# Kernel tuning notes

Measured on AMD Instinct MI355X. Metric: run time of the kernel, lower is better.

## Reference

```python
import jax, jax.numpy as jnp
import numpy as np

SPIN_LEN = 365
TRAIN_LEN = 200000
ML = 2.9086  # mean of second forcing (hard-coded in the torch module)
SL = 1.898   # std of second forcing (hard-coded in the torch module)


def setup_inputs() -> dict:
    key = jax.random.key(0)
    kx, ky, kp = jax.random.split(key, 3)
    B, S = 262144, 1
    x = jax.random.uniform(kx, (B, S, 2), dtype=jnp.float32)
    y_obs = jax.random.uniform(ky, (B, 1), dtype=jnp.float32)
    ks = jax.random.split(kp, 6)
    return {
        "x": x,
        "y_obs": y_obs,
        "epoch": 1,
        "time_lag": 0,
        "weight_r_yom": jax.random.uniform(ks[0], (1, 1), dtype=jnp.float32),
        "weight_r_yom_gw": jax.random.uniform(ks[1], (1, 1), dtype=jnp.float32),
        "weight_r_ylm": jax.random.uniform(ks[2], (1, 1), dtype=jnp.float32),
        "weight_r_yfm": jax.random.uniform(ks[3], (1, 1), dtype=jnp.float32),
        "bias_b0_ylm": jax.random.uniform(ks[4], (1,), dtype=jnp.float32),
        "weight_b2_ylm": jax.random.uniform(ks[5], (1, 1), dtype=jnp.float32),
    }


def reference(x, y_obs, epoch, time_lag, weight_r_yom, weight_r_yom_gw,
              weight_r_ylm, weight_r_yfm, bias_b0_ylm, weight_b2_ylm):
    # x: [B, S, 2] (batch_first). The torch code transposes to [S, B, 2] and
    # runs b-outer / t-inner loops with state threaded across BOTH loops, so
    # the scan order over flattened steps is b-major, t-minor.
    B, S, _ = x.shape
    dt = x.dtype

    # softmax-like mass-balance gate normalization over the 4 scalar weights
    e_om = jnp.exp(weight_r_yom[0, 0])
    e_gw = jnp.exp(weight_r_yom_gw[0, 0])
    e_lm = jnp.exp(weight_r_ylm[0, 0])
    e_fm = jnp.exp(weight_r_yfm[0, 0])
    denom = e_om + e_gw + e_lm + e_fm
    oo = e_om / denom      # constant output gate
    oogw = e_gw / denom    # constant groundwater gate
    ol1 = e_lm / denom     # loss-gate scale
    b0 = bias_b0_ylm[0]
    wb2 = weight_b2_ylm[0, 0]

    # unbiased std, matching torch.std default
    obsstd = jnp.std(y_obs[SPIN_LEN:TRAIN_LEN], ddof=1)

    xv = x[time_lag:]                       # [B', S, 2] (time_lag is static)
    Bp = B - time_lag
    u1 = xv[..., 0].reshape(-1)             # [B'*S] inflow
    u2 = xv[..., 1].reshape(-1)             # [B'*S] loss forcing

    def step(c, u):
        u1_t, u2_t = u
        ol = ol1 * jax.nn.sigmoid(b0 + (u2_t - ML) / SL * wb2)
        f = 1.0 - oo - ol - oogw
        c_new = f * c + u1_t                # ib = 0 -> full inflow enters
        return c_new, (c, ol, f)

    _, (c_prev, ol_s, f_s) = jax.lax.scan(step, jnp.zeros((), dt), (u1, u2))

    # torch stores outputs every t but overwrites; only last t per b survives,
    # using c_0 (state BEFORE that step) and that step's ol/f.
    c0 = c_prev.reshape(Bp, S)[:, -1]
    olL = ol_s.reshape(Bp, S)[:, -1]
    fL = f_s.reshape(Bp, S)[:, -1]

    def pad(v):  # rows b < time_lag stay zero, shape [B, 1]
        return jnp.pad(v, (time_lag, 0))[:, None]

    h_n = pad(oo * c0)          # bp = 0 so h_n == q_n
    c_n = pad(c0)
    l_n = pad(olL * c0)
    gw_n = pad(oogw * c0)
    bp_n = jnp.zeros((B, 1), dt)
    gate_ib = jnp.zeros((B, 1), dt)
    valid = pad(jnp.ones((Bp,), dt))
    gate_oo = oo * valid
    gate_oogw = oogw * valid
    gate_ol = pad(olL)
    gate_f = pad(fL)
    obs_std = obsstd * valid
    h_nout = jnp.concatenate([h_n, obs_std], axis=1)
    return (h_n, c_n, l_n, gw_n, bp_n, gate_ib, gate_oo, gate_oogw,
            gate_ol, gate_f, h_nout, obs_std)
```

## Files before the change

kernel.cpp:

```cpp
#include <hip/hip_runtime.h>
#include <math.h>

#define SPIN 365
#define TRAINL 200000

#define THREADS 256
#define ITEMS 4
#define CHUNK (THREADS * ITEMS)


struct Sc { float oo, oogw, ol1, b0, wb2; };

__device__ __forceinline__ Sc get_sc(const float* w0, const float* w1,
                                     const float* w2, const float* w3,
                                     const float* b0p, const float* wb2p) {
  float e_om = expf(w0[0]);
  float e_gw = expf(w1[0]);
  float e_lm = expf(w2[0]);
  float e_fm = expf(w3[0]);
  float denom = e_om + e_gw + e_lm + e_fm;
  Sc s;
  s.oo   = e_om / denom;
  s.oogw = e_gw / denom;
  s.ol1  = e_lm / denom;
  s.b0   = b0p[0];
  s.wb2  = wb2p[0];
  return s;
}

__device__ __forceinline__ float sigm(float z) { return 1.0f / (1.0f + expf(-z)); }


extern "C" __global__ __launch_bounds__(THREADS) void k_phase1(
    const float* __restrict__ x, const float* __restrict__ y,
    const int* __restrict__ tlp,
    const float* __restrict__ w0, const float* __restrict__ w1,
    const float* __restrict__ w2, const float* __restrict__ w3,
    const float* __restrict__ b0p, const float* __restrict__ wb2p,
    float* __restrict__ out, float* __restrict__ ws, int B, int G)
{
  const int g = blockIdx.x, tid = threadIdx.x;
  const int tl = tlp[0];
  const Sc sc = get_sc(w0, w1, w2, w3, b0p, wb2p);
  const int base = g * CHUNK + tid * ITEMS;
  const bool full = (base + ITEMS) <= B;

  float u1v[ITEMS], u2v[ITEMS];
  if (full) {
    float4 a = *(const float4*)(x + 2 * (size_t)base);
    float4 b = *(const float4*)(x + 2 * (size_t)base + 4);
    u1v[0]=a.x; u2v[0]=a.y; u1v[1]=a.z; u2v[1]=a.w;
    u1v[2]=b.x; u2v[2]=b.y; u1v[3]=b.z; u2v[3]=b.w;
  } else {
    for (int j = 0; j < ITEMS; j++) {
      int p = base + j;
      u1v[j] = (p < B) ? x[2*(size_t)p]     : 0.f;
      u2v[j] = (p < B) ? x[2*(size_t)p + 1] : 0.f;
    }
  }

  float P = 1.f, Q = 0.f;
  float voo[ITEMS], vgw[ITEMS], vol[ITEMS], vf[ITEMS];
  for (int j = 0; j < ITEMS; j++) {
    int p = base + j;
    float ol = sc.ol1 * sigm(sc.b0 + (u2v[j] - 2.9086f) / 1.898f * sc.wb2);
    float f  = 1.0f - sc.oo - ol - sc.oogw;
    bool act = (p >= tl) && (p < B);
    voo[j] = act ? sc.oo   : 0.f;
    vgw[j] = act ? sc.oogw : 0.f;
    vol[j] = act ? ol      : 0.f;
    vf[j]  = act ? f       : 0.f;
    if (act) { Q = f * Q + u1v[j]; P *= f; }
  }

  if (full) {
    *(float4*)(out + 4*(size_t)B + base) = make_float4(0,0,0,0);
    *(float4*)(out + 5*(size_t)B + base) = make_float4(0,0,0,0);
    *(float4*)(out + 6*(size_t)B + base) = make_float4(voo[0],voo[1],voo[2],voo[3]);
    *(float4*)(out + 7*(size_t)B + base) = make_float4(vgw[0],vgw[1],vgw[2],vgw[3]);
    *(float4*)(out + 8*(size_t)B + base) = make_float4(vol[0],vol[1],vol[2],vol[3]);
    *(float4*)(out + 9*(size_t)B + base) = make_float4(vf[0],vf[1],vf[2],vf[3]);
  } else {
    for (int j = 0; j < ITEMS; j++) {
      int p = base + j;
      if (p < B) {
        out[4*(size_t)B+p] = 0.f;    out[5*(size_t)B+p] = 0.f;
        out[6*(size_t)B+p] = voo[j]; out[7*(size_t)B+p] = vgw[j];
        out[8*(size_t)B+p] = vol[j]; out[9*(size_t)B+p] = vf[j];
      }
    }
  }

  __shared__ float sA[THREADS], sB[THREADS];
  sA[tid] = P; sB[tid] = Q;
  __syncthreads();
  for (int off = 1; off < THREADS; off <<= 1) {
    float a = sA[tid], b = sB[tid];
    float pa = 1.f, pb = 0.f;
    if (tid >= off) { pa = sA[tid - off]; pb = sB[tid - off]; }
    __syncthreads();
    sA[tid] = pa * a;
    sB[tid] = a * pb + b;
    __syncthreads();
  }
  if (tid == THREADS - 1) { ws[g] = sA[tid]; ws[G + g] = sB[tid]; }

  float s = 0.f, ss = 0.f;
  if (base < TRAINL) {
    if (full) {
      float4 yv = *(const float4*)(y + base);
      float vv[4] = { yv.x, yv.y, yv.z, yv.w };
      for (int j = 0; j < ITEMS; j++) {
        int p = base + j;
        if (p >= SPIN && p < TRAINL) { s += vv[j]; ss += vv[j]*vv[j]; }
      }
    } else {
      for (int j = 0; j < ITEMS; j++) {
        int p = base + j;
        if (p >= SPIN && p < TRAINL && p < B) { float v = y[p]; s += v; ss += v*v; }
      }
    }
  }
  __syncthreads();
  sA[tid] = s; sB[tid] = ss;
  __syncthreads();
  for (int off = THREADS/2; off > 0; off >>= 1) {
    if (tid < off) { sA[tid] += sA[tid + off]; sB[tid] += sB[tid + off]; }
    __syncthreads();
  }
  if (tid == 0) { ws[2*G + g] = sA[0]; ws[3*G + g] = sB[0]; }
}

extern "C" __global__ __launch_bounds__(THREADS) void k_phase2(
    float* __restrict__ ws, int G)
{
  const int tid = threadIdx.x;
  __shared__ float sA[THREADS], sB[THREADS];
  float a = (tid < G) ? ws[tid]     : 1.f;
  float b = (tid < G) ? ws[G + tid] : 0.f;
  sA[tid] = a; sB[tid] = b;
  __syncthreads();
  for (int off = 1; off < THREADS; off <<= 1) {
    float ca = sA[tid], cb = sB[tid];
    float pa = 1.f, pb = 0.f;
    if (tid >= off) { pa = sA[tid - off]; pb = sB[tid - off]; }
    __syncthreads();
    sA[tid] = pa * ca;
    sB[tid] = ca * pb + cb;
    __syncthreads();
  }
  if (tid < G) ws[4*G + tid] = (tid == 0) ? 0.f : sB[tid - 1];
  __syncthreads();

  float s  = (tid < G) ? ws[2*G + tid] : 0.f;
  float ss = (tid < G) ? ws[3*G + tid] : 0.f;
  sA[tid] = s; sB[tid] = ss;
  __syncthreads();
  for (int off = THREADS/2; off > 0; off >>= 1) {
    if (tid < off) { sA[tid] += sA[tid + off]; sB[tid] += sB[tid + off]; }
    __syncthreads();
  }
  if (tid == 0) {
    float n = (float)(TRAINL - SPIN);
    float S = sA[0], SS = sB[0];
    float mean = S / n;
    float var = (SS - n * mean * mean) / (n - 1.0f);
    ws[5*G] = sqrtf(fmaxf(var, 0.f));
  }
}

extern "C" __global__ __launch_bounds__(THREADS) void k_phase3(
    const float* __restrict__ x, const int* __restrict__ tlp,
    const float* __restrict__ w0, const float* __restrict__ w1,
    const float* __restrict__ w2, const float* __restrict__ w3,
    const float* __restrict__ b0p, const float* __restrict__ wb2p,
    float* __restrict__ out, const float* __restrict__ ws, int B, int G)
{
  const int g = blockIdx.x, tid = threadIdx.x;
  const int tl = tlp[0];
  const Sc sc = get_sc(w0, w1, w2, w3, b0p, wb2p);
  const int base = g * CHUNK + tid * ITEMS;
  const bool full = (base + ITEMS) <= B;

  float u1v[ITEMS], u2v[ITEMS];
  if (full) {
    float4 a = *(const float4*)(x + 2 * (size_t)base);
    float4 b = *(const float4*)(x + 2 * (size_t)base + 4);
    u1v[0]=a.x; u2v[0]=a.y; u1v[1]=a.z; u2v[1]=a.w;
    u1v[2]=b.x; u2v[2]=b.y; u1v[3]=b.z; u2v[3]=b.w;
  } else {
    for (int j = 0; j < ITEMS; j++) {
      int p = base + j;
      u1v[j] = (p < B) ? x[2*(size_t)p]     : 0.f;
      u2v[j] = (p < B) ? x[2*(size_t)p + 1] : 0.f;
    }
  }

  float P = 1.f, Q = 0.f;
  float fv[ITEMS], olv[ITEMS];
  for (int j = 0; j < ITEMS; j++) {
    int p = base + j;
    float ol = sc.ol1 * sigm(sc.b0 + (u2v[j] - 2.9086f) / 1.898f * sc.wb2);
    float f  = 1.0f - sc.oo - ol - sc.oogw;
    bool act = (p >= tl) && (p < B);
    olv[j] = ol; fv[j] = f;
    if (act) { Q = f * Q + u1v[j]; P *= f; }
  }

  __shared__ float sA[THREADS], sB[THREADS];
  sA[tid] = P; sB[tid] = Q;
  __syncthreads();
  for (int off = 1; off < THREADS; off <<= 1) {
    float a = sA[tid], b = sB[tid];
    float pa = 1.f, pb = 0.f;
    if (tid >= off) { pa = sA[tid - off]; pb = sB[tid - off]; }
    __syncthreads();
    sA[tid] = pa * a;
    sB[tid] = a * pb + b;
    __syncthreads();
  }
  float Ae = 1.f, Be = 0.f;
  if (tid > 0) { Ae = sA[tid - 1]; Be = sB[tid - 1]; }

  const float Cg   = ws[4*G + g];
  const float ostd = ws[5*G];
  float c = Ae * Cg + Be;

  float vh[ITEMS], vc[ITEMS], vl[ITEMS], vgw[ITEMS], vos[ITEMS];
  for (int j = 0; j < ITEMS; j++) {
    int p = base + j;
    bool act = (p >= tl) && (p < B);
    float c0 = c;
    vh[j]  = sc.oo * c0;
    vc[j]  = c0;
    vl[j]  = olv[j] * c0;
    vgw[j] = sc.oogw * c0;
    vos[j] = act ? ostd : 0.f;
    if (act) { c = fv[j] * c + u1v[j]; }
  }

  if (full) {
    *(float4*)(out + (size_t)base)            = make_float4(vh[0],vh[1],vh[2],vh[3]);
    *(float4*)(out + (size_t)B + base)        = make_float4(vc[0],vc[1],vc[2],vc[3]);
    *(float4*)(out + 2*(size_t)B + base)      = make_float4(vl[0],vl[1],vl[2],vl[3]);
    *(float4*)(out + 3*(size_t)B + base)      = make_float4(vgw[0],vgw[1],vgw[2],vgw[3]);
    *(float4*)(out + 12*(size_t)B + base)     = make_float4(vos[0],vos[1],vos[2],vos[3]);
    *(float4*)(out + 10*(size_t)B + 2*base)     = make_float4(vh[0],vos[0],vh[1],vos[1]);
    *(float4*)(out + 10*(size_t)B + 2*base + 4) = make_float4(vh[2],vos[2],vh[3],vos[3]);
  } else {
    for (int j = 0; j < ITEMS; j++) {
      int p = base + j;
      if (p < B) {
        out[(size_t)p]            = vh[j];
        out[(size_t)B + p]        = vc[j];
        out[2*(size_t)B + p]      = vl[j];
        out[3*(size_t)B + p]      = vgw[j];
        out[12*(size_t)B + p]     = vos[j];
        out[10*(size_t)B + 2*p]     = vh[j];
        out[10*(size_t)B + 2*p + 1] = vos[j];
      }
    }
  }
}

extern "C" void kernel_launch(void* const* d_in, const int* in_sizes, int n_in,
                              void* d_out, int out_size, void* d_ws, size_t ws_size,
                              hipStream_t stream) {
  const float* x   = (const float*)d_in[0];
  const float* y   = (const float*)d_in[1];
  const int*   tl  = (const int*)d_in[3];
  const float* w0  = (const float*)d_in[4];
  const float* w1  = (const float*)d_in[5];
  const float* w2  = (const float*)d_in[6];
  const float* w3  = (const float*)d_in[7];
  const float* b0  = (const float*)d_in[8];
  const float* wb2 = (const float*)d_in[9];

  float* out = (float*)d_out;
  float* ws  = (float*)d_ws;

  const int B = in_sizes[0] / 2;
  const int G = (B + CHUNK - 1) / CHUNK;

  k_phase1<<<G, THREADS, 0, stream>>>(x, y, tl, w0, w1, w2, w3, b0, wb2, out, ws, B, G);
  k_phase2<<<1, THREADS, 0, stream>>>(ws, G);
  k_phase3<<<G, THREADS, 0, stream>>>(x, tl, w0, w1, w2, w3, b0, wb2, out, ws, B, G);
}
```

Before: 85.90 us.

## Fuse three scan phases into one kernel with grid-wide atomic barrier

Replaces the three-kernel scan (local scan, single-block carry scan, apply pass) with one persistent kernel. Blocks publish their aggregates, wait on an atomic counter until all G blocks arrive, then each block redundantly scans the block aggregates and reduces the std sums itself. This removes two kernel launches and the reload and recompute of x in the third phase. In exchange it adds a memset launch and a spin barrier, which relies on all 256 blocks being co-resident.

```diff
diff --git a/kernel.cpp b/kernel.cpp
--- a/kernel.cpp
+++ b/kernel.cpp
@@ -7,7 +7,6 @@
 #define THREADS 256
 #define ITEMS 4
 #define CHUNK (THREADS * ITEMS)
-
 
 struct Sc { float oo, oogw, ol1, b0, wb2; };
 
@@ -31,13 +30,14 @@
 __device__ __forceinline__ float sigm(float z) { return 1.0f / (1.0f + expf(-z)); }
 
 
-extern "C" __global__ __launch_bounds__(THREADS) void k_phase1(
+extern "C" __global__ __launch_bounds__(THREADS) void k_fused(
     const float* __restrict__ x, const float* __restrict__ y,
     const int* __restrict__ tlp,
     const float* __restrict__ w0, const float* __restrict__ w1,
     const float* __restrict__ w2, const float* __restrict__ w3,
     const float* __restrict__ b0p, const float* __restrict__ wb2p,
-    float* __restrict__ out, float* __restrict__ ws, int B, int G)
+    float* __restrict__ out, float* __restrict__ ws,
+    unsigned int* __restrict__ cnt, int B, int G)
 {
   const int g = blockIdx.x, tid = threadIdx.x;
   const int tl = tlp[0];
@@ -60,20 +60,26 @@
   }
 
   float P = 1.f, Q = 0.f;
-  float voo[ITEMS], vgw[ITEMS], vol[ITEMS], vf[ITEMS];
+  float olv[ITEMS], fv[ITEMS];
   for (int j = 0; j < ITEMS; j++) {
     int p = base + j;
     float ol = sc.ol1 * sigm(sc.b0 + (u2v[j] - 2.9086f) / 1.898f * sc.wb2);
     float f  = 1.0f - sc.oo - ol - sc.oogw;
+    olv[j] = ol; fv[j] = f;
     bool act = (p >= tl) && (p < B);
-    voo[j] = act ? sc.oo   : 0.f;
-    vgw[j] = act ? sc.oogw : 0.f;
-    vol[j] = act ? ol      : 0.f;
-    vf[j]  = act ? f       : 0.f;
     if (act) { Q = f * Q + u1v[j]; P *= f; }
   }
 
   if (full) {
+    float voo[ITEMS], vgw[ITEMS], vol[ITEMS], vf[ITEMS];
+    for (int j = 0; j < ITEMS; j++) {
+      int p = base + j;
+      bool act = (p >= tl);
+      voo[j] = act ? sc.oo   : 0.f;
+      vgw[j] = act ? sc.oogw : 0.f;
+      vol[j] = act ? olv[j]  : 0.f;
+      vf[j]  = act ? fv[j]   : 0.f;
+    }
     *(float4*)(out + 4*(size_t)B + base) = make_float4(0,0,0,0);
     *(float4*)(out + 5*(size_t)B + base) = make_float4(0,0,0,0);
     *(float4*)(out + 6*(size_t)B + base) = make_float4(voo[0],voo[1],voo[2],voo[3]);
@@ -84,9 +90,10 @@
     for (int j = 0; j < ITEMS; j++) {
       int p = base + j;
       if (p < B) {
-        out[4*(size_t)B+p] = 0.f;    out[5*(size_t)B+p] = 0.f;
-        out[6*(size_t)B+p] = voo[j]; out[7*(size_t)B+p] = vgw[j];
-        out[8*(size_t)B+p] = vol[j]; out[9*(size_t)B+p] = vf[j];
+        bool act = (p >= tl);
+        out[4*(size_t)B+p] = 0.f;                     out[5*(size_t)B+p] = 0.f;
+        out[6*(size_t)B+p] = act ? sc.oo   : 0.f;     out[7*(size_t)B+p] = act ? sc.oogw : 0.f;
+        out[8*(size_t)B+p] = act ? olv[j]  : 0.f;     out[9*(size_t)B+p] = act ? fv[j]   : 0.f;
       }
     }
   }
@@ -103,7 +110,10 @@
     sB[tid] = a * pb + b;
     __syncthreads();
   }
+  float Ae = 1.f, Be = 0.f;
+  if (tid > 0) { Ae = sA[tid - 1]; Be = sB[tid - 1]; }
   if (tid == THREADS - 1) { ws[g] = sA[tid]; ws[G + g] = sB[tid]; }
+  __syncthreads();
 
   float s = 0.f, ss = 0.f;
   if (base < TRAINL) {
@@ -121,7 +131,6 @@
       }
     }
   }
-  __syncthreads();
   sA[tid] = s; sB[tid] = ss;
   __syncthreads();
   for (int off = THREADS/2; off > 0; off >>= 1) {
@@ -129,103 +138,54 @@
     __syncthreads();
   }
   if (tid == 0) { ws[2*G + g] = sA[0]; ws[3*G + g] = sB[0]; }
-}
-
-extern "C" __global__ __launch_bounds__(THREADS) void k_phase2(
-    float* __restrict__ ws, int G)
-{
-  const int tid = threadIdx.x;
-  __shared__ float sA[THREADS], sB[THREADS];
-  float a = (tid < G) ? ws[tid]     : 1.f;
-  float b = (tid < G) ? ws[G + tid] : 0.f;
-  sA[tid] = a; sB[tid] = b;
+
+  __threadfence();
+  __syncthreads();
+  if (tid == 0) {
+    __hip_atomic_fetch_add(cnt, 1u, __ATOMIC_ACQ_REL, __HIP_MEMORY_SCOPE_AGENT);
+    while (__hip_atomic_load(cnt, __ATOMIC_ACQUIRE, __HIP_MEMORY_SCOPE_AGENT) < (unsigned)G) {
+      __builtin_amdgcn_s_sleep(2);
+    }
+  }
+  __syncthreads();
+
+  float aP = 1.f, aQ = 0.f, yS = 0.f, ySS = 0.f;
+  if (tid < G) {
+    aP  = __hip_atomic_load(&ws[tid],       __ATOMIC_RELAXED, __HIP_MEMORY_SCOPE_AGENT);
+    aQ  = __hip_atomic_load(&ws[G + tid],   __ATOMIC_RELAXED, __HIP_MEMORY_SCOPE_AGENT);
+    yS  = __hip_atomic_load(&ws[2*G + tid], __ATOMIC_RELAXED, __HIP_MEMORY_SCOPE_AGENT);
+    ySS = __hip_atomic_load(&ws[3*G + tid], __ATOMIC_RELAXED, __HIP_MEMORY_SCOPE_AGENT);
+  }
+  sA[tid] = aP; sB[tid] = aQ;
   __syncthreads();
   for (int off = 1; off < THREADS; off <<= 1) {
-    float ca = sA[tid], cb = sB[tid];
+    float a = sA[tid], b = sB[tid];
     float pa = 1.f, pb = 0.f;
     if (tid >= off) { pa = sA[tid - off]; pb = sB[tid - off]; }
     __syncthreads();
-    sA[tid] = pa * ca;
-    sB[tid] = ca * pb + cb;
-    __syncthreads();
-  }
-  if (tid < G) ws[4*G + tid] = (tid == 0) ? 0.f : sB[tid - 1];
-  __syncthreads();
-
-  float s  = (tid < G) ? ws[2*G + tid] : 0.f;
-  float ss = (tid < G) ? ws[3*G + tid] : 0.f;
-  sA[tid] = s; sB[tid] = ss;
+    sA[tid] = pa * a;
+    sB[tid] = a * pb + b;
+    __syncthreads();
+  }
+  const float Cg = (g == 0) ? 0.f : sB[g - 1];
+  __syncthreads();
+
+  sA[tid] = yS; sB[tid] = ySS;
   __syncthreads();
   for (int off = THREADS/2; off > 0; off >>= 1) {
     if (tid < off) { sA[tid] += sA[tid + off]; sB[tid] += sB[tid + off]; }
     __syncthreads();
   }
-  if (tid == 0) {
+  float ostd;
+  {
     float n = (float)(TRAINL - SPIN);
     float S = sA[0], SS = sB[0];
     float mean = S / n;
     float var = (SS - n * mean * mean) / (n - 1.0f);
-    ws[5*G] = sqrtf(fmaxf(var, 0.f));
-  }
-}
-
-extern "C" __global__ __launch_bounds__(THREADS) void k_phase3(
-    const float* __restrict__ x, const int* __restrict__ tlp,
-    const float* __restrict__ w0, const float* __restrict__ w1,
-    const float* __restrict__ w2, const float* __restrict__ w3,
-    const float* __restrict__ b0p, const float* __restrict__ wb2p,
-    float* __restrict__ out, const float* __restrict__ ws, int B, int G)
-{
-  const int g = blockIdx.x, tid = threadIdx.x;
-  const int tl = tlp[0];
-  const Sc sc = get_sc(w0, w1, w2, w3, b0p, wb2p);
-  const int base = g * CHUNK + tid * ITEMS;
-  const bool full = (base + ITEMS) <= B;
-
-  float u1v[ITEMS], u2v[ITEMS];
-  if (full) {
-    float4 a = *(const float4*)(x + 2 * (size_t)base);
-    float4 b = *(const float4*)(x + 2 * (size_t)base + 4);
-    u1v[0]=a.x; u2v[0]=a.y; u1v[1]=a.z; u2v[1]=a.w;
-    u1v[2]=b.x; u2v[2]=b.y; u1v[3]=b.z; u2v[3]=b.w;
-  } else {
-    for (int j = 0; j < ITEMS; j++) {
-      int p = base + j;
-      u1v[j] = (p < B) ? x[2*(size_t)p]     : 0.f;
-      u2v[j] = (p < B) ? x[2*(size_t)p + 1] : 0.f;
-    }
-  }
-
-  float P = 1.f, Q = 0.f;
-  float fv[ITEMS], olv[ITEMS];
-  for (int j = 0; j < ITEMS; j++) {
-    int p = base + j;
-    float ol = sc.ol1 * sigm(sc.b0 + (u2v[j] - 2.9086f) / 1.898f * sc.wb2);
-    float f  = 1.0f - sc.oo - ol - sc.oogw;
-    bool act = (p >= tl) && (p < B);
-    olv[j] = ol; fv[j] = f;
-    if (act) { Q = f * Q + u1v[j]; P *= f; }
-  }
-
-  __shared__ float sA[THREADS], sB[THREADS];
-  sA[tid] = P; sB[tid] = Q;
-  __syncthreads();
-  for (int off = 1; off < THREADS; off <<= 1) {
-    float a = sA[tid], b = sB[tid];
-    float pa = 1.f, pb = 0.f;
-    if (tid >= off) { pa = sA[tid - off]; pb = sB[tid - off]; }
-    __syncthreads();
-    sA[tid] = pa * a;
-    sB[tid] = a * pb + b;
-    __syncthreads();
-  }
-  float Ae = 1.f, Be = 0.f;
-  if (tid > 0) { Ae = sA[tid - 1]; Be = sB[tid - 1]; }
-
-  const float Cg   = ws[4*G + g];
-  const float ostd = ws[5*G];
+    ostd = sqrtf(fmaxf(var, 0.f));
+  }
+
   float c = Ae * Cg + Be;
-
   float vh[ITEMS], vc[ITEMS], vl[ITEMS], vgw[ITEMS], vos[ITEMS];
   for (int j = 0; j < ITEMS; j++) {
     int p = base + j;
@@ -240,11 +200,11 @@
   }
 
   if (full) {
-    *(float4*)(out + (size_t)base)            = make_float4(vh[0],vh[1],vh[2],vh[3]);
-    *(float4*)(out + (size_t)B + base)        = make_float4(vc[0],vc[1],vc[2],vc[3]);
-    *(float4*)(out + 2*(size_t)B + base)      = make_float4(vl[0],vl[1],vl[2],vl[3]);
-    *(float4*)(out + 3*(size_t)B + base)      = make_float4(vgw[0],vgw[1],vgw[2],vgw[3]);
-    *(float4*)(out + 12*(size_t)B + base)     = make_float4(vos[0],vos[1],vos[2],vos[3]);
+    *(float4*)(out + (size_t)base)        = make_float4(vh[0],vh[1],vh[2],vh[3]);
+    *(float4*)(out + (size_t)B + base)    = make_float4(vc[0],vc[1],vc[2],vc[3]);
+    *(float4*)(out + 2*(size_t)B + base)  = make_float4(vl[0],vl[1],vl[2],vl[3]);
+    *(float4*)(out + 3*(size_t)B + base)  = make_float4(vgw[0],vgw[1],vgw[2],vgw[3]);
+    *(float4*)(out + 12*(size_t)B + base) = make_float4(vos[0],vos[1],vos[2],vos[3]);
     *(float4*)(out + 10*(size_t)B + 2*base)     = make_float4(vh[0],vos[0],vh[1],vos[1]);
     *(float4*)(out + 10*(size_t)B + 2*base + 4) = make_float4(vh[2],vos[2],vh[3],vos[3]);
   } else {
@@ -282,7 +242,9 @@
   const int B = in_sizes[0] / 2;
   const int G = (B + CHUNK - 1) / CHUNK;
 
-  k_phase1<<<G, THREADS, 0, stream>>>(x, y, tl, w0, w1, w2, w3, b0, wb2, out, ws, B, G);
-  k_phase2<<<1, THREADS, 0, stream>>>(ws, G);
-  k_phase3<<<G, THREADS, 0, stream>>>(x, tl, w0, w1, w2, w3, b0, wb2, out, ws, B, G);
+  unsigned int* cnt = (unsigned int*)(ws + 4 * (size_t)G);
+  hipMemsetAsync(cnt, 0, sizeof(unsigned int), stream);
+
+  k_fused<<<G, THREADS, 0, stream>>>(x, y, tl, w0, w1, w2, w3, b0, wb2,
+                                     out, ws, cnt, B, G);
 }
```

Result: slower. 104.6 us (+21.8%).

## Fold block-aggregate scan into output kernel and use wavefront shuffle scans

Applied to the files above, without the earlier changes.

Removes the single-block middle kernel. Each output block now redundantly scans all per-block (P,Q) aggregates and y-sums with wavefront shuffles, so the carry-in and the obs std are computed locally. The shared-memory Hillis-Steele scans and tree reductions, with a barrier at every step, are replaced by 64-lane __shfl_up/__shfl_xor scans plus a short per-wave combine. The block becomes 512 threads with 2 items each, and fast __expf/__fdividef is used for the sigmoid. The risks are redundant aggregate work in every block, a hard limit of G at most THREADS, and a small change in sigmoid precision.

```diff
diff --git a/kernel.cpp b/kernel.cpp
--- a/kernel.cpp
+++ b/kernel.cpp
@@ -3,35 +3,39 @@
 
 #define SPIN 365
 #define TRAINL 200000
-
-#define THREADS 256
-#define ITEMS 4
+#define ML 2.9086f
+#define SLINV (1.0f / 1.898f)
+
+#define THREADS 512
+#define ITEMS 2
 #define CHUNK (THREADS * ITEMS)
-
-
-struct Sc { float oo, oogw, ol1, b0, wb2; };
+#define NW (THREADS / 64)
+
+struct Sc { float oo, oogw, ol1, b0, k; };
 
 __device__ __forceinline__ Sc get_sc(const float* w0, const float* w1,
                                      const float* w2, const float* w3,
                                      const float* b0p, const float* wb2p) {
-  float e_om = expf(w0[0]);
-  float e_gw = expf(w1[0]);
-  float e_lm = expf(w2[0]);
-  float e_fm = expf(w3[0]);
+  float e_om = __expf(w0[0]);
+  float e_gw = __expf(w1[0]);
+  float e_lm = __expf(w2[0]);
+  float e_fm = __expf(w3[0]);
   float denom = e_om + e_gw + e_lm + e_fm;
   Sc s;
   s.oo   = e_om / denom;
   s.oogw = e_gw / denom;
   s.ol1  = e_lm / denom;
   s.b0   = b0p[0];
-  s.wb2  = wb2p[0];
+  s.k    = wb2p[0] * SLINV;
   return s;
 }
 
-__device__ __forceinline__ float sigm(float z) { return 1.0f / (1.0f + expf(-z)); }
-
-
-extern "C" __global__ __launch_bounds__(THREADS) void k_phase1(
+__device__ __forceinline__ float sigm_fast(float z) {
+  return __fdividef(1.0f, 1.0f + __expf(-z));
+}
+
+
+extern "C" __global__ __launch_bounds__(THREADS) void k1(
     const float* __restrict__ x, const float* __restrict__ y,
     const int* __restrict__ tlp,
     const float* __restrict__ w0, const float* __restrict__ w1,
@@ -40,6 +44,7 @@
     float* __restrict__ out, float* __restrict__ ws, int B, int G)
 {
   const int g = blockIdx.x, tid = threadIdx.x;
+  const int lane = tid & 63, wid = tid >> 6;
   const int tl = tlp[0];
   const Sc sc = get_sc(w0, w1, w2, w3, b0p, wb2p);
   const int base = g * CHUNK + tid * ITEMS;
@@ -48,9 +53,7 @@
   float u1v[ITEMS], u2v[ITEMS];
   if (full) {
     float4 a = *(const float4*)(x + 2 * (size_t)base);
-    float4 b = *(const float4*)(x + 2 * (size_t)base + 4);
-    u1v[0]=a.x; u2v[0]=a.y; u1v[1]=a.z; u2v[1]=a.w;
-    u1v[2]=b.x; u2v[2]=b.y; u1v[3]=b.z; u2v[3]=b.w;
+    u1v[0] = a.x; u2v[0] = a.y; u1v[1] = a.z; u2v[1] = a.w;
   } else {
     for (int j = 0; j < ITEMS; j++) {
       int p = base + j;
@@ -60,116 +63,80 @@
   }
 
   float P = 1.f, Q = 0.f;
-  float voo[ITEMS], vgw[ITEMS], vol[ITEMS], vf[ITEMS];
+  float olv[ITEMS], fv[ITEMS];
   for (int j = 0; j < ITEMS; j++) {
     int p = base + j;
-    float ol = sc.ol1 * sigm(sc.b0 + (u2v[j] - 2.9086f) / 1.898f * sc.wb2);
+    float ol = sc.ol1 * sigm_fast(sc.b0 + (u2v[j] - ML) * sc.k);
     float f  = 1.0f - sc.oo - ol - sc.oogw;
+    olv[j] = ol; fv[j] = f;
     bool act = (p >= tl) && (p < B);
-    voo[j] = act ? sc.oo   : 0.f;
-    vgw[j] = act ? sc.oogw : 0.f;
-    vol[j] = act ? ol      : 0.f;
-    vf[j]  = act ? f       : 0.f;
     if (act) { Q = f * Q + u1v[j]; P *= f; }
   }
 
   if (full) {
-    *(float4*)(out + 4*(size_t)B + base) = make_float4(0,0,0,0);
-    *(float4*)(out + 5*(size_t)B + base) = make_float4(0,0,0,0);
-    *(float4*)(out + 6*(size_t)B + base) = make_float4(voo[0],voo[1],voo[2],voo[3]);
-    *(float4*)(out + 7*(size_t)B + base) = make_float4(vgw[0],vgw[1],vgw[2],vgw[3]);
-    *(float4*)(out + 8*(size_t)B + base) = make_float4(vol[0],vol[1],vol[2],vol[3]);
-    *(float4*)(out + 9*(size_t)B + base) = make_float4(vf[0],vf[1],vf[2],vf[3]);
+    bool a0 = (base >= tl), a1 = (base + 1 >= tl);
+    *(float2*)(out + 4*(size_t)B + base) = make_float2(0.f, 0.f);
+    *(float2*)(out + 5*(size_t)B + base) = make_float2(0.f, 0.f);
+    *(float2*)(out + 6*(size_t)B + base) = make_float2(a0?sc.oo:0.f,  a1?sc.oo:0.f);
+    *(float2*)(out + 7*(size_t)B + base) = make_float2(a0?sc.oogw:0.f,a1?sc.oogw:0.f);
+    *(float2*)(out + 8*(size_t)B + base) = make_float2(a0?olv[0]:0.f, a1?olv[1]:0.f);
+    *(float2*)(out + 9*(size_t)B + base) = make_float2(a0?fv[0]:0.f,  a1?fv[1]:0.f);
   } else {
     for (int j = 0; j < ITEMS; j++) {
       int p = base + j;
       if (p < B) {
-        out[4*(size_t)B+p] = 0.f;    out[5*(size_t)B+p] = 0.f;
-        out[6*(size_t)B+p] = voo[j]; out[7*(size_t)B+p] = vgw[j];
-        out[8*(size_t)B+p] = vol[j]; out[9*(size_t)B+p] = vf[j];
+        bool act = (p >= tl);
+        out[4*(size_t)B+p] = 0.f;                  out[5*(size_t)B+p] = 0.f;
+        out[6*(size_t)B+p] = act ? sc.oo   : 0.f;  out[7*(size_t)B+p] = act ? sc.oogw : 0.f;
+        out[8*(size_t)B+p] = act ? olv[j]  : 0.f;  out[9*(size_t)B+p] = act ? fv[j]   : 0.f;
       }
     }
   }
 
-  __shared__ float sA[THREADS], sB[THREADS];
-  sA[tid] = P; sB[tid] = Q;
+  #pragma unroll
+  for (int off = 1; off < 64; off <<= 1) {
+    float pL = __shfl_down(P, off);
+    float qL = __shfl_down(Q, off);
+    Q = pL * Q + qL;
+    P = pL * P;
+  }
+
+  float s = 0.f, ss = 0.f;
+  if (full && base < TRAINL) {
+    float2 yv = *(const float2*)(y + base);
+    float vv[2] = { yv.x, yv.y };
+    for (int j = 0; j < ITEMS; j++) {
+      int p = base + j;
+      if (p >= SPIN && p < TRAINL) { s += vv[j]; ss += vv[j]*vv[j]; }
+    }
+  } else {
+    for (int j = 0; j < ITEMS; j++) {
+      int p = base + j;
+      if (p >= SPIN && p < TRAINL && p < B) { float v = y[p]; s += v; ss += v*v; }
+    }
+  }
+  #pragma unroll
+  for (int off = 1; off < 64; off <<= 1) {
+    s  += __shfl_xor(s,  off);
+    ss += __shfl_xor(ss, off);
+  }
+
+  __shared__ float wA[NW], wB[NW], rS[NW], rSS[NW];
+  if (lane == 0) { wA[wid] = P; wB[wid] = Q; rS[wid] = s; rSS[wid] = ss; }
   __syncthreads();
-  for (int off = 1; off < THREADS; off <<= 1) {
-    float a = sA[tid], b = sB[tid];
-    float pa = 1.f, pb = 0.f;
-    if (tid >= off) { pa = sA[tid - off]; pb = sB[tid - off]; }
-    __syncthreads();
-    sA[tid] = pa * a;
-    sB[tid] = a * pb + b;
-    __syncthreads();
-  }
-  if (tid == THREADS - 1) { ws[g] = sA[tid]; ws[G + g] = sB[tid]; }
-
-  float s = 0.f, ss = 0.f;
-  if (base < TRAINL) {
-    if (full) {
-      float4 yv = *(const float4*)(y + base);
-      float vv[4] = { yv.x, yv.y, yv.z, yv.w };
-      for (int j = 0; j < ITEMS; j++) {
-        int p = base + j;
-        if (p >= SPIN && p < TRAINL) { s += vv[j]; ss += vv[j]*vv[j]; }
-      }
-    } else {
-      for (int j = 0; j < ITEMS; j++) {
-        int p = base + j;
-        if (p >= SPIN && p < TRAINL && p < B) { float v = y[p]; s += v; ss += v*v; }
-      }
-    }
-  }
-  __syncthreads();
-  sA[tid] = s; sB[tid] = ss;
-  __syncthreads();
-  for (int off = THREADS/2; off > 0; off >>= 1) {
-    if (tid < off) { sA[tid] += sA[tid + off]; sB[tid] += sB[tid + off]; }
-    __syncthreads();
-  }
-  if (tid == 0) { ws[2*G + g] = sA[0]; ws[3*G + g] = sB[0]; }
-}
-
-extern "C" __global__ __launch_bounds__(THREADS) void k_phase2(
-    float* __restrict__ ws, int G)
-{
-  const int tid = threadIdx.x;
-  __shared__ float sA[THREADS], sB[THREADS];
-  float a = (tid < G) ? ws[tid]     : 1.f;
-  float b = (tid < G) ? ws[G + tid] : 0.f;
-  sA[tid] = a; sB[tid] = b;
-  __syncthreads();
-  for (int off = 1; off < THREADS; off <<= 1) {
-    float ca = sA[tid], cb = sB[tid];
-    float pa = 1.f, pb = 0.f;
-    if (tid >= off) { pa = sA[tid - off]; pb = sB[tid - off]; }
-    __syncthreads();
-    sA[tid] = pa * ca;
-    sB[tid] = ca * pb + cb;
-    __syncthreads();
-  }
-  if (tid < G) ws[4*G + tid] = (tid == 0) ? 0.f : sB[tid - 1];
-  __syncthreads();
-
-  float s  = (tid < G) ? ws[2*G + tid] : 0.f;
-  float ss = (tid < G) ? ws[3*G + tid] : 0.f;
-  sA[tid] = s; sB[tid] = ss;
-  __syncthreads();
-  for (int off = THREADS/2; off > 0; off >>= 1) {
-    if (tid < off) { sA[tid] += sA[tid + off]; sB[tid] += sB[tid + off]; }
-    __syncthreads();
-  }
   if (tid == 0) {
-    float n = (float)(TRAINL - SPIN);
-    float S = sA[0], SS = sB[0];
-    float mean = S / n;
-    float var = (SS - n * mean * mean) / (n - 1.0f);
-    ws[5*G] = sqrtf(fmaxf(var, 0.f));
-  }
-}
-
-extern "C" __global__ __launch_bounds__(THREADS) void k_phase3(
+    float A = 1.f, Bq = 0.f, S = 0.f, SS = 0.f;
+    #pragma unroll
+    for (int w = 0; w < NW; w++) {
+      Bq = wA[w] * Bq + wB[w];
+      A  = wA[w] * A;
+      S += rS[w]; SS += rSS[w];
+    }
+    ws[g] = A; ws[G + g] = Bq; ws[2*G + g] = S; ws[3*G + g] = SS;
+  }
+}
+
+extern "C" __global__ __launch_bounds__(THREADS) void k2(
     const float* __restrict__ x, const int* __restrict__ tlp,
     const float* __restrict__ w0, const float* __restrict__ w1,
     const float* __restrict__ w2, const float* __restrict__ w3,
@@ -177,6 +144,7 @@
     float* __restrict__ out, const float* __restrict__ ws, int B, int G)
 {
   const int g = blockIdx.x, tid = threadIdx.x;
+  const int lane = tid & 63, wid = tid >> 6;
   const int tl = tlp[0];
   const Sc sc = get_sc(w0, w1, w2, w3, b0p, wb2p);
   const int base = g * CHUNK + tid * ITEMS;
@@ -185,9 +153,7 @@
   float u1v[ITEMS], u2v[ITEMS];
   if (full) {
     float4 a = *(const float4*)(x + 2 * (size_t)base);
-    float4 b = *(const float4*)(x + 2 * (size_t)base + 4);
-    u1v[0]=a.x; u2v[0]=a.y; u1v[1]=a.z; u2v[1]=a.w;
-    u1v[2]=b.x; u2v[2]=b.y; u1v[3]=b.z; u2v[3]=b.w;
+    u1v[0] = a.x; u2v[0] = a.y; u1v[1] = a.z; u2v[1] = a.w;
   } else {
     for (int j = 0; j < ITEMS; j++) {
       int p = base + j;
@@ -195,37 +161,77 @@
       u2v[j] = (p < B) ? x[2*(size_t)p + 1] : 0.f;
     }
   }
-
   float P = 1.f, Q = 0.f;
-  float fv[ITEMS], olv[ITEMS];
+  float olv[ITEMS], fv[ITEMS];
   for (int j = 0; j < ITEMS; j++) {
     int p = base + j;
-    float ol = sc.ol1 * sigm(sc.b0 + (u2v[j] - 2.9086f) / 1.898f * sc.wb2);
+    float ol = sc.ol1 * sigm_fast(sc.b0 + (u2v[j] - ML) * sc.k);
     float f  = 1.0f - sc.oo - ol - sc.oogw;
+    olv[j] = ol; fv[j] = f;
     bool act = (p >= tl) && (p < B);
-    olv[j] = ol; fv[j] = f;
     if (act) { Q = f * Q + u1v[j]; P *= f; }
   }
 
-  __shared__ float sA[THREADS], sB[THREADS];
-  sA[tid] = P; sB[tid] = Q;
+  float iP = P, iQ = Q;
+  #pragma unroll
+  for (int off = 1; off < 64; off <<= 1) {
+    float pa = __shfl_up(iP, off);
+    float pb = __shfl_up(iQ, off);
+    if (lane >= off) { iQ = iP * pb + iQ; iP = iP * pa; }
+  }
+
+  float aP  = (tid < G) ? ws[tid]       : 1.f;
+  float aQ  = (tid < G) ? ws[G + tid]   : 0.f;
+  float ys  = (tid < G) ? ws[2*G + tid] : 0.f;
+  float yss = (tid < G) ? ws[3*G + tid] : 0.f;
+
+  float jP = aP, jQ = aQ;
+  #pragma unroll
+  for (int off = 1; off < 64; off <<= 1) {
+    float pa = __shfl_up(jP, off);
+    float pb = __shfl_up(jQ, off);
+    if (lane >= off) { jQ = jP * pb + jQ; jP = jP * pa; }
+  }
+
+  #pragma unroll
+  for (int off = 1; off < 64; off <<= 1) {
+    ys  += __shfl_xor(ys,  off);
+    yss += __shfl_xor(yss, off);
+  }
+
+  __shared__ float wOA[NW], wOB[NW];
+  __shared__ float wAA[NW], wAB[NW];
+  __shared__ float rS[NW], rSS[NW];
+  __shared__ float sQ[THREADS];
+  if (lane == 63) { wOA[wid] = iP; wOB[wid] = iQ; wAA[wid] = jP; wAB[wid] = jQ; }
+  if (lane == 0)  { rS[wid] = ys; rSS[wid] = yss; }
   __syncthreads();
-  for (int off = 1; off < THREADS; off <<= 1) {
-    float a = sA[tid], b = sB[tid];
-    float pa = 1.f, pb = 0.f;
-    if (tid >= off) { pa = sA[tid - off]; pb = sB[tid - off]; }
-    __syncthreads();
-    sA[tid] = pa * a;
-    sB[tid] = a * pb + b;
-    __syncthreads();
-  }
-  float Ae = 1.f, Be = 0.f;
-  if (tid > 0) { Ae = sA[tid - 1]; Be = sB[tid - 1]; }
-
-  const float Cg   = ws[4*G + g];
-  const float ostd = ws[5*G];
+
+  float OWA = 1.f, OWB = 0.f, AWA = 1.f, AWB = 0.f;
+  for (int w = 0; w < wid; w++) {
+    OWB = wOA[w] * OWB + wOB[w];  OWA = wOA[w] * OWA;
+    AWB = wAA[w] * AWB + wAB[w];  AWA = wAA[w] * AWA;
+  }
+  sQ[tid] = jP * AWB + jQ;
+
+  float S = 0.f, SS = 0.f;
+  #pragma unroll
+  for (int w = 0; w < NW; w++) { S += rS[w]; SS += rSS[w]; }
+  float n = (float)(TRAINL - SPIN);
+  float mean = S / n;
+  float var = (SS - n * mean * mean) / (n - 1.0f);
+  float ostd = sqrtf(fmaxf(var, 0.f));
+  __syncthreads();
+
+  const float Cg = (g == 0) ? 0.f : sQ[g - 1];
+
+  float eP = __shfl_up(iP, 1);
+  float eQ = __shfl_up(iQ, 1);
+  if (lane == 0) { eP = 1.f; eQ = 0.f; }
+  float Ae = eP * OWA;
+  float Be = eP * OWB + eQ;
+
   float c = Ae * Cg + Be;
-
   float vh[ITEMS], vc[ITEMS], vl[ITEMS], vgw[ITEMS], vos[ITEMS];
   for (int j = 0; j < ITEMS; j++) {
     int p = base + j;
@@ -240,13 +246,12 @@
   }
 
   if (full) {
-    *(float4*)(out + (size_t)base)            = make_float4(vh[0],vh[1],vh[2],vh[3]);
-    *(float4*)(out + (size_t)B + base)        = make_float4(vc[0],vc[1],vc[2],vc[3]);
-    *(float4*)(out + 2*(size_t)B + base)      = make_float4(vl[0],vl[1],vl[2],vl[3]);
-    *(float4*)(out + 3*(size_t)B + base)      = make_float4(vgw[0],vgw[1],vgw[2],vgw[3]);
-    *(float4*)(out + 12*(size_t)B + base)     = make_float4(vos[0],vos[1],vos[2],vos[3]);
-    *(float4*)(out + 10*(size_t)B + 2*base)     = make_float4(vh[0],vos[0],vh[1],vos[1]);
-    *(float4*)(out + 10*(size_t)B + 2*base + 4) = make_float4(vh[2],vos[2],vh[3],vos[3]);
+    *(float2*)(out + (size_t)base)        = make_float2(vh[0], vh[1]);
+    *(float2*)(out + (size_t)B + base)    = make_float2(vc[0], vc[1]);
+    *(float2*)(out + 2*(size_t)B + base)  = make_float2(vl[0], vl[1]);
+    *(float2*)(out + 3*(size_t)B + base)  = make_float2(vgw[0], vgw[1]);
+    *(float2*)(out + 12*(size_t)B + base) = make_float2(vos[0], vos[1]);
+    *(float4*)(out + 10*(size_t)B + 2*(size_t)base) = make_float4(vh[0], vos[0], vh[1], vos[1]);
   } else {
     for (int j = 0; j < ITEMS; j++) {
       int p = base + j;
@@ -282,7 +287,6 @@
   const int B = in_sizes[0] / 2;
   const int G = (B + CHUNK - 1) / CHUNK;
 
-  k_phase1<<<G, THREADS, 0, stream>>>(x, y, tl, w0, w1, w2, w3, b0, wb2, out, ws, B, G);
-  k_phase2<<<1, THREADS, 0, stream>>>(ws, G);
-  k_phase3<<<G, THREADS, 0, stream>>>(x, tl, w0, w1, w2, w3, b0, wb2, out, ws, B, G);
-}
+  k1<<<G, THREADS, 0, stream>>>(x, y, tl, w0, w1, w2, w3, b0, wb2, out, ws, B, G);
+  k2<<<G, THREADS, 0, stream>>>(x, tl, w0, w1, w2, w3, b0, wb2, out, ws, B, G);
+}
```

Result: faster. 80.31 us (-6.5%).
